# Optimization experiments

Measured on AMD Instinct MI355X. Metric: run time of the kernel, lower is better.

The kernel has to match this reference:

```python
import jax, jax.numpy as jnp
import numpy as np

EPS = 1e-5  # torch InstanceNorm3d default eps


def setup_inputs() -> dict:
    key = jax.random.key(0)
    ks = jax.random.split(key, 7)
    B, C, H, W, D = 2, 128, 48, 48, 48
    c_m, c_n = 128, 64
    return {
        "x": jax.random.normal(ks[0], (B, C, H, W, D), dtype=jnp.float32),
        "WA": jax.random.normal(ks[1], (c_m, C), dtype=jnp.float32) * (1.0 / np.sqrt(C)),
        "bA": jax.random.normal(ks[2], (c_m,), dtype=jnp.float32) * 0.01,
        "WB": jax.random.normal(ks[3], (c_n, C), dtype=jnp.float32) * (1.0 / np.sqrt(C)),
        "bB": jax.random.normal(ks[4], (c_n,), dtype=jnp.float32) * 0.01,
        "WV": jax.random.normal(ks[5], (c_n, C), dtype=jnp.float32) * (1.0 / np.sqrt(C)),
        "bV": jax.random.normal(ks[6], (c_n,), dtype=jnp.float32) * 0.01,
    }


def reference(x, WA, bA, WB, bB, WV, bV):
    B, C, H, W, D = x.shape
    L = H * W * D
    xf = x.reshape(B, C, L)
    # 1x1x1 Conv3d projections == per-voxel linear over channels
    A = jnp.einsum('bcl,mc->bml', xf, WA) + bA[None, :, None]   # (B, c_m, L)
    Bm = jnp.einsum('bcl,nc->bnl', xf, WB) + bB[None, :, None]  # (B, c_n, L)
    V = jnp.einsum('bcl,nc->bnl', xf, WV) + bV[None, :, None]   # (B, c_n, L)
    # attention maps: softmax over spatial positions
    attn_maps = jax.nn.softmax(Bm, axis=-1)                     # (B, c_n, L)
    # global descriptors: A @ attn_maps^T
    G = jnp.einsum('bml,bnl->bmn', A, attn_maps)                # (B, c_m, c_n)
    # attention vectors: softmax over c_n (channel) dim
    attn_vec = jax.nn.softmax(V, axis=1)                        # (B, c_n, L)
    Z = jnp.einsum('bmn,bnl->bml', G, attn_vec)                 # (B, c_m, L)
    # InstanceNorm3d (affine=False, biased variance) per (batch, channel)
    mean = jnp.mean(Z, axis=-1, keepdims=True)
    var = jnp.var(Z, axis=-1, keepdims=True)
    Zn = (Z - mean) * jax.lax.rsqrt(var + EPS)
    return Zn.reshape(B, Z.shape[1], H, W, D)
```

## Files before the change

### kernel.cpp

```cpp
#include <hip/hip_runtime.h>

#define LTOT 110592
#define EPSV 1e-5f

typedef _Float16 f16;
typedef __attribute__((ext_vector_type(4))) _Float16 f16x4;
typedef __attribute__((ext_vector_type(8))) _Float16 f16x8;
typedef __attribute__((ext_vector_type(4))) float f32x4;

#define MFMA16(a, b, c) __builtin_amdgcn_mfma_f32_16x16x32_f16(a, b, c, 0, 0, 0)
#define SWC(c) ((((c) ^ ((c) >> 3)) & 7) << 3)

__device__ __forceinline__ f16x8 ld_w8(const float* p) {
  const float4 a = *(const float4*)p;
  const float4 b = *(const float4*)(p + 4);
  f16x8 f;
  f[0] = (f16)a.x; f[1] = (f16)a.y; f[2] = (f16)a.z; f[3] = (f16)a.w;
  f[4] = (f16)b.x; f[5] = (f16)b.y; f[6] = (f16)b.z; f[7] = (f16)b.w;
  return f;
}

__global__ __launch_bounds__(256, 2) void p1_proj_m(
    const float* __restrict__ x,
    const float* __restrict__ WB_, const float* __restrict__ bB_,
    const float* __restrict__ WV_, const float* __restrict__ bV_,
    f16* __restrict__ av_g, f16* __restrict__ mpart, float* __restrict__ separt)
{
  __shared__ __align__(16) f16 XT[64 * 128 + 2240];
  __shared__ __align__(16) f16 XC[128 * 64];
  __shared__ __align__(16) f16 EL[64 * 64];
  __shared__ __align__(16) f16 AVT[64 * 64];
  __shared__ float colp[4][64];
  const int tid = threadIdx.x, b = blockIdx.y, blk = blockIdx.x;
  const int ln = tid & 63, w = tid >> 6, g = ln >> 4;

  const int nB = w * 16 + (ln & 15);
  f16x8 wbf[4], wvf[4];
  #pragma unroll
  for (int ks = 0; ks < 4; ++ks) {
    wbf[ks] = ld_w8(&WB_[nB * 128 + ks * 32 + g * 8]);
    wvf[ks] = ld_w8(&WV_[nB * 128 + ks * 32 + g * 8]);
  }
  const float sB = bB_[nB];
  float biasV[4];
  #pragma unroll
  for (int r = 0; r < 4; ++r) biasV[r] = bV_[w * 16 + g * 4 + r];

  f32x4 macc[8];
  #pragma unroll
  for (int i = 0; i < 8; ++i) macc[i] = (f32x4){0.f, 0.f, 0.f, 0.f};
  float se = 0.f;

  const int co = tid >> 4, LQ = tid & 15;
  const size_t xb = (size_t)b * 128 * LTOT;

  float4 xr[8];
  {
    const int l0 = blk * 256;
    #pragma unroll
    for (int j = 0; j < 8; ++j)
      xr[j] = *(const float4*)&x[xb + (size_t)(co * 8 + j) * LTOT + l0 + LQ * 4];
  }

  for (int t = 0; t < 4; ++t) {
    const int l0 = (blk * 4 + t) * 64;
    __syncthreads();
    #pragma unroll
    for (int i = 0; i < 4; ++i) {
      const int l = LQ * 4 + i;
      f16x8 v;
      #pragma unroll
      for (int j = 0; j < 8; ++j) v[j] = (f16)(((const float*)&xr[j])[i]);
      *(f16x8*)&XT[l * 128 + ((co * 8) ^ ((l & 7) << 3))] = v;
    }
    #pragma unroll
    for (int j = 0; j < 8; ++j) {
      const int c = co * 8 + j;
      f16x4 q;
      q[0] = (f16)xr[j].x; q[1] = (f16)xr[j].y;
      q[2] = (f16)xr[j].z; q[3] = (f16)xr[j].w;
      *(f16x4*)&XC[c * 64 + ((LQ * 4) ^ SWC(c))] = q;
    }
    __syncthreads();
    if (t < 3) {
      const int l0n = l0 + 64;
      #pragma unroll
      for (int j = 0; j < 8; ++j)
        xr[j] = *(const float4*)&x[xb + (size_t)(co * 8 + j) * LTOT + l0n + LQ * 4];
    }
    f32x4 aB[4], aV[4];
    #pragma unroll
    for (int lt = 0; lt < 4; ++lt) {
      aB[lt] = (f32x4){0.f, 0.f, 0.f, 0.f};
      aV[lt] = (f32x4){0.f, 0.f, 0.f, 0.f};
      const int l = lt * 16 + (ln & 15);
      #pragma unroll
      for (int ks = 0; ks < 4; ++ks) {
        const f16x8 xf = *(const f16x8*)&XT[l * 128 + (((ks * 4 + g) * 8) ^ ((l & 7) << 3))];
        aB[lt] = MFMA16(xf, wbf[ks], aB[lt]);
        aV[lt] = MFMA16(wvf[ks], xf, aV[lt]);
      }
    }
    #pragma unroll
    for (int lt = 0; lt < 4; ++lt) {
      f16x4 ev4;
      #pragma unroll
      for (int r = 0; r < 4; ++r) {
        const float e = __expf(aB[lt][r] + sB);
        se += e;
        ev4[r] = (f16)e;
      }
      const int lq = lt * 16 + g * 4;
      *(f16x4*)&EL[nB * 64 + (lq ^ ((nB & 7) << 3))] = ev4;
    }
    float cs[4];
    #pragma unroll
    for (int ct = 0; ct < 4; ++ct) {
      f16x4 av4;
      float s = 0.f;
      #pragma unroll
      for (int r = 0; r < 4; ++r) {
        const float e = __expf(aV[ct][r] + biasV[r]);
        s += e;
        av4[r] = (f16)e;
      }
      cs[ct] = s;
      const int l = ct * 16 + (ln & 15);
      *(f16x4*)&AVT[l * 64 + ((w * 16 + g * 4) ^ ((l & 7) << 3))] = av4;
    }
    #pragma unroll
    for (int ct = 0; ct < 4; ++ct) {
      cs[ct] += __shfl_xor(cs[ct], 16);
      cs[ct] += __shfl_xor(cs[ct], 32);
    }
    {
      const float v = (g == 0) ? cs[0] : (g == 1) ? cs[1] : (g == 2) ? cs[2] : cs[3];
      colp[w][g * 16 + (ln & 15)] = v;
    }
    __syncthreads();
    {
      const int l = tid >> 2, q = tid & 3;
      const float rs = 1.f / (colp[0][l] + colp[1][l] + colp[2][l] + colp[3][l]);
      f16x8 a0 = *(const f16x8*)&AVT[l * 64 + ((q * 16) ^ ((l & 7) << 3))];
      f16x8 a1 = *(const f16x8*)&AVT[l * 64 + ((q * 16 + 8) ^ ((l & 7) << 3))];
      #pragma unroll
      for (int j = 0; j < 8; ++j) {
        a0[j] = (f16)((float)a0[j] * rs);
        a1[j] = (f16)((float)a1[j] * rs);
      }
      f16* gp = av_g + ((size_t)b * LTOT + l0 + l) * 64 + q * 16;
      *(f16x8*)&gp[0] = a0;
      *(f16x8*)&gp[8] = a1;
    }
    {
      f16x8 el[2];
      #pragma unroll
      for (int ks = 0; ks < 2; ++ks)
        el[ks] = *(const f16x8*)&EL[nB * 64 + ((ks * 32 + g * 8) ^ ((nB & 7) << 3))];
      #pragma unroll
      for (int cblk = 0; cblk < 8; ++cblk) {
        const int c = cblk * 16 + (ln & 15);
        #pragma unroll
        for (int ks = 0; ks < 2; ++ks) {
          const f16x8 xcf = *(const f16x8*)&XC[c * 64 + ((ks * 32 + g * 8) ^ SWC(c))];
          macc[cblk] = MFMA16(el[ks], xcf, macc[cblk]);
        }
      }
    }
  }
  f16* mp = mpart + (size_t)(b * 432 + blk) * 8192;
  #pragma unroll
  for (int cblk = 0; cblk < 8; ++cblk)
    #pragma unroll
    for (int r = 0; r < 4; ++r)
      mp[(w * 16 + g * 4 + r) * 128 + cblk * 16 + (ln & 15)] = (f16)macc[cblk][r];
  se += __shfl_xor(se, 16);
  se += __shfl_xor(se, 32);
  if (ln < 16) separt[(size_t)(b * 432 + blk) * 64 + w * 16 + ln] = se;
}

__global__ __launch_bounds__(256, 2) void ka_red_cov(
    const f16* __restrict__ mpart, const float* __restrict__ separt,
    float* __restrict__ mpart2, float* __restrict__ sesum,
    const f16* __restrict__ av_g, f16* __restrict__ cpart,
    float* __restrict__ mupart)
{
  __shared__ __align__(16) f16 AV[64 * 64];
  const int bxa = blockIdx.x, b = blockIdx.y, tid = threadIdx.x;
  if (bxa < 257) {
    const int bx = bxa;
    if (bx < 256) {
      const int seg = bx >> 5, chunk = bx & 31;
      const int idx = chunk * 256 + tid;
      float s = 0.f;
      for (int j = 0; j < 54; ++j)
        s += (float)mpart[(size_t)(b * 432 + seg * 54 + j) * 8192 + idx];
      mpart2[(size_t)(b * 8 + seg) * 8192 + idx] = s;
    } else if (tid < 64) {
      float s = 0.f;
      for (int k = 0; k < 432; ++k) s += separt[(size_t)(b * 432 + k) * 64 + tid];
      sesum[b * 64 + tid] = s;
    }
    return;
  }
  const int blk = bxa - 257;
  const int ln = tid & 63, w = tid >> 6, g = ln >> 4;
  const int nq4 = (tid & 15) * 4, lq4 = (tid >> 4) * 4;
  const int nmu = tid >> 2, qmu = tid & 3;

  f32x4 cacc[4];
  #pragma unroll
  for (int j = 0; j < 4; ++j) cacc[j] = (f32x4){0.f, 0.f, 0.f, 0.f};
  float muacc = 0.f;

  for (int t = 0; t < 8; ++t) {
    const int l0 = (blk * 8 + t) * 64;
    __syncthreads();
    {
      f16x4 rd[4];
      #pragma unroll
      for (int i = 0; i < 4; ++i)
        rd[i] = *(const f16x4*)&av_g[((size_t)b * LTOT + l0 + lq4 + i) * 64 + nq4];
      #pragma unroll
      for (int j = 0; j < 4; ++j) {
        const int n = nq4 + j;
        f16x4 wr;
        #pragma unroll
        for (int i = 0; i < 4; ++i) wr[i] = rd[i][j];
        *(f16x4*)&AV[n * 64 + (lq4 ^ ((n & 7) << 3))] = wr;
      }
    }
    __syncthreads();
    {
      const f16x8 a0 = *(const f16x8*)&AV[nmu * 64 + ((qmu * 16) ^ ((nmu & 7) << 3))];
      const f16x8 a1 = *(const f16x8*)&AV[nmu * 64 + ((qmu * 16 + 8) ^ ((nmu & 7) << 3))];
      #pragma unroll
      for (int j = 0; j < 8; ++j) muacc += (float)a0[j] + (float)a1[j];
    }
    const int nA = w * 16 + (ln & 15);
    f16x8 caf[2];
    #pragma unroll
    for (int ks = 0; ks < 2; ++ks)
      caf[ks] = *(const f16x8*)&AV[nA * 64 + ((ks * 32 + g * 8) ^ ((nA & 7) << 3))];
    #pragma unroll
    for (int nct = 0; nct < 4; ++nct) {
      const int nb = nct * 16 + (ln & 15);
      #pragma unroll
      for (int ks = 0; ks < 2; ++ks) {
        const f16x8 cbf = *(const f16x8*)&AV[nb * 64 + ((ks * 32 + g * 8) ^ ((nb & 7) << 3))];
        cacc[nct] = MFMA16(caf[ks], cbf, cacc[nct]);
      }
    }
  }
  f16* cp = cpart + (size_t)(b * 216 + blk) * 4096;
  #pragma unroll
  for (int nct = 0; nct < 4; ++nct)
    #pragma unroll
    for (int r = 0; r < 4; ++r)
      cp[(w * 16 + g * 4 + r) * 64 + nct * 16 + (ln & 15)] = (f16)cacc[nct][r];
  muacc += __shfl_xor(muacc, 1);
  muacc += __shfl_xor(muacc, 2);
  if (qmu == 0) mupart[(size_t)(b * 216 + blk) * 64 + nmu] = muacc;
}

__global__ void kb_red(const float* __restrict__ mpart2, float* __restrict__ msum,
                       const f16* __restrict__ cpart, const float* __restrict__ mupart,
                       float* __restrict__ csum, float* __restrict__ musum)
{
  const int bxa = blockIdx.x, b = blockIdx.y, tid = threadIdx.x;
  if (bxa < 32) {
    const int idx = bxa * 256 + tid;
    float s = 0.f;
    #pragma unroll
    for (int k = 0; k < 8; ++k) s += mpart2[(size_t)(b * 8 + k) * 8192 + idx];
    msum[(size_t)b * 8192 + idx] = s;
    return;
  }
  const int bx = bxa - 32;
  if (bx < 64) {
    const int idx = bx * 64 + (tid >> 2), q = tid & 3;
    float s = 0.f;
    for (int k = q; k < 216; k += 4) s += (float)cpart[(size_t)(b * 216 + k) * 4096 + idx];
    s += __shfl_xor(s, 1);
    s += __shfl_xor(s, 2);
    if (q == 0) csum[(size_t)b * 4096 + idx] = s;
  } else if (tid < 64) {
    float s = 0.f;
    for (int k = 0; k < 216; ++k) s += mupart[(size_t)(b * 216 + k) * 64 + tid];
    musum[b * 64 + tid] = s;
  }
}

__global__ void p2b(const float* __restrict__ WA_, const float* __restrict__ bA_,
                    const float* __restrict__ msum, const float* __restrict__ sesum,
                    float* __restrict__ g32, f16* __restrict__ g16)
{
  const int b = blockIdx.y;
  const int idx = blockIdx.x * 256 + threadIdx.x;
  const int m = idx >> 6, n = idx & 63;
  float s = 0.f;
  #pragma unroll 4
  for (int c = 0; c < 128; ++c) s += WA_[m * 128 + c] * msum[(size_t)b * 8192 + n * 128 + c];
  const float gv = s / sesum[b * 64 + n] + bA_[m];
  g32[(size_t)b * 8192 + m * 64 + n] = gv;
  g16[(size_t)b * 8192 + m * 64 + (n ^ ((m & 7) << 3))] = (f16)gv;
}

__global__ void p4b(const float* __restrict__ csum, const float* __restrict__ musum,
                    const float* __restrict__ g32, float* __restrict__ mr)
{
  __shared__ __align__(16) float CL[4096];
  __shared__ __align__(16) float GLs[32 * 68];
  __shared__ float MUL[64];
  const int tid = threadIdx.x, b = blockIdx.y, bx = blockIdx.x;
  #pragma unroll
  for (int k = 0; k < 16; ++k) CL[k * 256 + tid] = csum[(size_t)b * 4096 + k * 256 + tid];
  #pragma unroll
  for (int k = 0; k < 8; ++k) {
    const int idx = k * 256 + tid;
    const int m_ = idx >> 6, n_ = idx & 63;
    GLs[m_ * 68 + n_] = g32[(size_t)b * 8192 + (bx * 32 + m_) * 64 + n_];
  }
  if (tid < 64) MUL[tid] = musum[b * 64 + tid];
  __syncthreads();
  const int mrow = (tid >> 3) * 68, oct = tid & 7;
  float q = 0.f;
  #pragma unroll
  for (int q4 = 0; q4 < 2; ++q4) {
    const int npb = oct * 8 + q4 * 4;
    float t0 = 0.f, t1 = 0.f, t2 = 0.f, t3 = 0.f;
    #pragma unroll 8
    for (int n = 0; n < 64; ++n) {
      const float4 cv = *(const float4*)&CL[n * 64 + npb];
      const float gv = GLs[mrow + n];
      t0 += gv * cv.x; t1 += gv * cv.y; t2 += gv * cv.z; t3 += gv * cv.w;
    }
    const float4 gq = *(const float4*)&GLs[mrow + npb];
    q += t0 * gq.x + t1 * gq.y + t2 * gq.z + t3 * gq.w;
  }
  q += __shfl_xor(q, 1); q += __shfl_xor(q, 2); q += __shfl_xor(q, 4);
  if (oct == 0) {
    float meanq = 0.f;
    #pragma unroll 8
    for (int n = 0; n < 64; ++n) meanq += GLs[mrow + n] * MUL[n];
    const int m = bx * 32 + (tid >> 3);
    const float mean = meanq / (float)LTOT;
    const float var = fmaxf(q / (float)LTOT - mean * mean, 0.f);
    mr[(b * 128 + m) * 2] = mean;
    mr[(b * 128 + m) * 2 + 1] = rsqrtf(var + EPSV);
  }
}

__global__ __launch_bounds__(256, 2) void p5_z(
    const f16* __restrict__ av_g, const f16* __restrict__ g16,
    const float* __restrict__ mr, float* __restrict__ out)
{
  __shared__ __align__(16) f16 AVT[64 * 64];
  const int tid = threadIdx.x, b = blockIdx.y, blk = blockIdx.x;
  const int ln = tid & 63, w = tid >> 6, g = ln >> 4;
  const int lst = tid & 63, pst = tid >> 6;

  f16x8 gf[2][2];
  float mean_[2][4], rsig_[2][4];
  #pragma unroll
  for (int mct = 0; mct < 2; ++mct) {
    const int mA = w * 32 + mct * 16 + (ln & 15);
    #pragma unroll
    for (int ks = 0; ks < 2; ++ks)
      gf[mct][ks] = *(const f16x8*)&g16[(size_t)b * 8192 + mA * 64 +
                                        (((ks * 4 + g) * 8) ^ ((mA & 7) << 3))];
    #pragma unroll
    for (int r = 0; r < 4; ++r) {
      const int m = w * 32 + mct * 16 + g * 4 + r;
      mean_[mct][r] = mr[(b * 128 + m) * 2];
      rsig_[mct][r] = mr[(b * 128 + m) * 2 + 1];
    }
  }

  for (int t = 0; t < 4; ++t) {
    const int l0 = (blk * 4 + t) * 64;
    __syncthreads();
    {
      const f16* gp = av_g + ((size_t)b * LTOT + l0 + lst) * 64 + pst * 16;
      const f16x8 a0 = *(const f16x8*)&gp[0];
      const f16x8 a1 = *(const f16x8*)&gp[8];
      *(f16x8*)&AVT[lst * 64 + ((pst * 16) ^ ((lst & 7) << 3))] = a0;
      *(f16x8*)&AVT[lst * 64 + ((pst * 16 + 8) ^ ((lst & 7) << 3))] = a1;
    }
    __syncthreads();
    #pragma unroll
    for (int lt = 0; lt < 4; ++lt) {
      const int l = lt * 16 + (ln & 15);
      f16x8 avf[2];
      #pragma unroll
      for (int ks = 0; ks < 2; ++ks)
        avf[ks] = *(const f16x8*)&AVT[l * 64 + (((ks * 4 + g) * 8) ^ ((l & 7) << 3))];
      #pragma unroll
      for (int mct = 0; mct < 2; ++mct) {
        f32x4 z = {0.f, 0.f, 0.f, 0.f};
        #pragma unroll
        for (int ks = 0; ks < 2; ++ks) z = MFMA16(gf[mct][ks], avf[ks], z);
        #pragma unroll
        for (int r = 0; r < 4; ++r) {
          const int m = w * 32 + mct * 16 + g * 4 + r;
          out[(size_t)(b * 128 + m) * LTOT + l0 + l] =
              (z[r] - mean_[mct][r]) * rsig_[mct][r];
        }
      }
    }
  }
}

extern "C" void kernel_launch(void* const* d_in, const int* in_sizes, int n_in,
                              void* d_out, int out_size, void* d_ws, size_t ws_size,
                              hipStream_t stream)
{
  const float* x  = (const float*)d_in[0];
  const float* WA = (const float*)d_in[1];
  const float* bA = (const float*)d_in[2];
  const float* WB = (const float*)d_in[3];
  const float* bB = (const float*)d_in[4];
  const float* WV = (const float*)d_in[5];
  const float* bV = (const float*)d_in[6];
  float* out = (float*)d_out;

  float* w = (float*)d_ws;
  f16*   mpart  = (f16*)w;
  float* mpart2 = w + 7077888;
  float* separt = mpart2 + 131072;
  float* msum   = separt + 55296;
  float* sesum  = msum + 16384;
  float* g32    = sesum + 128;
  f16*   g16f   = (f16*)(g32 + 16384);
  f16*   av_g   = g16f + 16384;
  f16*   cpart  = (f16*)(av_g + 14155776);
  float* mupart = (float*)(av_g + 14155776) + 1769472;
  float* csum   = mupart + 27648;
  float* musum  = csum + 8192;
  float* mr     = musum + 128;

  p1_proj_m<<<dim3(432, 2), 256, 0, stream>>>(x, WB, bB, WV, bV, av_g, mpart, separt);
  ka_red_cov<<<dim3(473, 2), 256, 0, stream>>>(mpart, separt, mpart2, sesum,
                                               av_g, cpart, mupart);
  kb_red<<<dim3(97, 2), 256, 0, stream>>>(mpart2, msum, cpart, mupart, csum, musum);
  p2b<<<dim3(32, 2), 256, 0, stream>>>(WA, bA, msum, sesum, g32, g16f);
  p4b<<<dim3(4, 2), 256, 0, stream>>>(csum, musum, g32, mr);
  p5_z<<<dim3(432, 2), 256, 0, stream>>>(av_g, g16f, mr, out);
}
```

Measured before the change: 110.3 us.

## Split p1 projection work across 512 threads with halved per-wave tiles

The first projection kernel now runs 512 threads per block. Each pair of waves shares one 16-row n slice and splits the spatial tiles and the channel blocks of the m accumulation between them. Per-thread register arrays (x prefetch, accumulators) are halved, which is meant to raise occupancy and latency hiding. The cost is more waves per block and doubled separt partial output, with the reduction and workspace offsets adjusted to match.

```diff
diff --git a/kernel.cpp b/kernel.cpp
--- a/kernel.cpp
+++ b/kernel.cpp
@@ -20,7 +20,7 @@
   return f;
 }
 
-__global__ __launch_bounds__(256, 2) void p1_proj_m(
+__global__ __launch_bounds__(512, 2) void p1_proj_m(
     const float* __restrict__ x,
     const float* __restrict__ WB_, const float* __restrict__ bB_,
     const float* __restrict__ WV_, const float* __restrict__ bV_,
@@ -33,8 +33,9 @@
   __shared__ float colp[4][64];
   const int tid = threadIdx.x, b = blockIdx.y, blk = blockIdx.x;
   const int ln = tid & 63, w = tid >> 6, g = ln >> 4;
-
-  const int nB = w * 16 + (ln & 15);
+  const int wn = w >> 1, h = w & 1;
+
+  const int nB = wn * 16 + (ln & 15);
   f16x8 wbf[4], wvf[4];
   #pragma unroll
   for (int ks = 0; ks < 4; ++ks) {
@@ -44,22 +45,22 @@
   const float sB = bB_[nB];
   float biasV[4];
   #pragma unroll
-  for (int r = 0; r < 4; ++r) biasV[r] = bV_[w * 16 + g * 4 + r];
-
-  f32x4 macc[8];
-  #pragma unroll
-  for (int i = 0; i < 8; ++i) macc[i] = (f32x4){0.f, 0.f, 0.f, 0.f};
+  for (int r = 0; r < 4; ++r) biasV[r] = bV_[wn * 16 + g * 4 + r];
+
+  f32x4 macc[4];
+  #pragma unroll
+  for (int i = 0; i < 4; ++i) macc[i] = (f32x4){0.f, 0.f, 0.f, 0.f};
   float se = 0.f;
 
-  const int co = tid >> 4, LQ = tid & 15;
+  const int cg = tid >> 4, LQ = tid & 15;
   const size_t xb = (size_t)b * 128 * LTOT;
 
-  float4 xr[8];
+  float4 xr[4];
   {
     const int l0 = blk * 256;
     #pragma unroll
-    for (int j = 0; j < 8; ++j)
-      xr[j] = *(const float4*)&x[xb + (size_t)(co * 8 + j) * LTOT + l0 + LQ * 4];
+    for (int j = 0; j < 4; ++j)
+      xr[j] = *(const float4*)&x[xb + (size_t)(cg * 4 + j) * LTOT + l0 + LQ * 4];
   }
 
   for (int t = 0; t < 4; ++t) {
@@ -68,14 +69,14 @@
     #pragma unroll
     for (int i = 0; i < 4; ++i) {
       const int l = LQ * 4 + i;
-      f16x8 v;
-      #pragma unroll
-      for (int j = 0; j < 8; ++j) v[j] = (f16)(((const float*)&xr[j])[i]);
-      *(f16x8*)&XT[l * 128 + ((co * 8) ^ ((l & 7) << 3))] = v;
-    }
-    #pragma unroll
-    for (int j = 0; j < 8; ++j) {
-      const int c = co * 8 + j;
+      f16x4 v;
+      #pragma unroll
+      for (int j = 0; j < 4; ++j) v[j] = (f16)(((const float*)&xr[j])[i]);
+      *(f16x4*)&XT[l * 128 + ((cg * 4) ^ ((l & 7) << 3))] = v;
+    }
+    #pragma unroll
+    for (int j = 0; j < 4; ++j) {
+      const int c = cg * 4 + j;
       f16x4 q;
       q[0] = (f16)xr[j].x; q[1] = (f16)xr[j].y;
       q[2] = (f16)xr[j].z; q[3] = (f16)xr[j].w;
@@ -85,72 +86,63 @@
     if (t < 3) {
       const int l0n = l0 + 64;
       #pragma unroll
-      for (int j = 0; j < 8; ++j)
-        xr[j] = *(const float4*)&x[xb + (size_t)(co * 8 + j) * LTOT + l0n + LQ * 4];
-    }
-    f32x4 aB[4], aV[4];
-    #pragma unroll
-    for (int lt = 0; lt < 4; ++lt) {
-      aB[lt] = (f32x4){0.f, 0.f, 0.f, 0.f};
-      aV[lt] = (f32x4){0.f, 0.f, 0.f, 0.f};
-      const int l = lt * 16 + (ln & 15);
+      for (int j = 0; j < 4; ++j)
+        xr[j] = *(const float4*)&x[xb + (size_t)(cg * 4 + j) * LTOT + l0n + LQ * 4];
+    }
+    f32x4 aB[2], aV[2];
+    #pragma unroll
+    for (int u = 0; u < 2; ++u) {
+      aB[u] = (f32x4){0.f, 0.f, 0.f, 0.f};
+      aV[u] = (f32x4){0.f, 0.f, 0.f, 0.f};
+      const int l = (2 * h + u) * 16 + (ln & 15);
       #pragma unroll
       for (int ks = 0; ks < 4; ++ks) {
         const f16x8 xf = *(const f16x8*)&XT[l * 128 + (((ks * 4 + g) * 8) ^ ((l & 7) << 3))];
-        aB[lt] = MFMA16(xf, wbf[ks], aB[lt]);
-        aV[lt] = MFMA16(wvf[ks], xf, aV[lt]);
-      }
-    }
-    #pragma unroll
-    for (int lt = 0; lt < 4; ++lt) {
+        aB[u] = MFMA16(xf, wbf[ks], aB[u]);
+        aV[u] = MFMA16(wvf[ks], xf, aV[u]);
+      }
+    }
+    #pragma unroll
+    for (int u = 0; u < 2; ++u) {
       f16x4 ev4;
       #pragma unroll
       for (int r = 0; r < 4; ++r) {
-        const float e = __expf(aB[lt][r] + sB);
+        const float e = __expf(aB[u][r] + sB);
         se += e;
         ev4[r] = (f16)e;
       }
-      const int lq = lt * 16 + g * 4;
+      const int lq = (2 * h + u) * 16 + g * 4;
       *(f16x4*)&EL[nB * 64 + (lq ^ ((nB & 7) << 3))] = ev4;
     }
-    float cs[4];
-    #pragma unroll
-    for (int ct = 0; ct < 4; ++ct) {
+    float cs[2];
+    #pragma unroll
+    for (int u = 0; u < 2; ++u) {
       f16x4 av4;
       float s = 0.f;
       #pragma unroll
       for (int r = 0; r < 4; ++r) {
-        const float e = __expf(aV[ct][r] + biasV[r]);
+        const float e = __expf(aV[u][r] + biasV[r]);
         s += e;
         av4[r] = (f16)e;
       }
-      cs[ct] = s;
-      const int l = ct * 16 + (ln & 15);
-      *(f16x4*)&AVT[l * 64 + ((w * 16 + g * 4) ^ ((l & 7) << 3))] = av4;
-    }
-    #pragma unroll
-    for (int ct = 0; ct < 4; ++ct) {
-      cs[ct] += __shfl_xor(cs[ct], 16);
-      cs[ct] += __shfl_xor(cs[ct], 32);
-    }
+      cs[u] = s;
+      const int l = (2 * h + u) * 16 + (ln & 15);
+      *(f16x4*)&AVT[l * 64 + ((wn * 16 + g * 4) ^ ((l & 7) << 3))] = av4;
+    }
+    #pragma unroll
+    for (int u = 0; u < 2; ++u) {
+      cs[u] += __shfl_xor(cs[u], 16);
+      cs[u] += __shfl_xor(cs[u], 32);
+    }
+    if (g < 2) colp[wn][(2 * h + g) * 16 + (ln & 15)] = cs[g & 1];
+    __syncthreads();
     {
-      const float v = (g == 0) ? cs[0] : (g == 1) ? cs[1] : (g == 2) ? cs[2] : cs[3];
-      colp[w][g * 16 + (ln & 15)] = v;
-    }
-    __syncthreads();
-    {
-      const int l = tid >> 2, q = tid & 3;
+      const int l = tid >> 3, q = tid & 7;
       const float rs = 1.f / (colp[0][l] + colp[1][l] + colp[2][l] + colp[3][l]);
-      f16x8 a0 = *(const f16x8*)&AVT[l * 64 + ((q * 16) ^ ((l & 7) << 3))];
-      f16x8 a1 = *(const f16x8*)&AVT[l * 64 + ((q * 16 + 8) ^ ((l & 7) << 3))];
-      #pragma unroll
-      for (int j = 0; j < 8; ++j) {
-        a0[j] = (f16)((float)a0[j] * rs);
-        a1[j] = (f16)((float)a1[j] * rs);
-      }
-      f16* gp = av_g + ((size_t)b * LTOT + l0 + l) * 64 + q * 16;
-      *(f16x8*)&gp[0] = a0;
-      *(f16x8*)&gp[8] = a1;
+      f16x8 a0 = *(const f16x8*)&AVT[l * 64 + ((q * 8) ^ ((l & 7) << 3))];
+      #pragma unroll
+      for (int j = 0; j < 8; ++j) a0[j] = (f16)((float)a0[j] * rs);
+      *(f16x8*)&av_g[((size_t)b * LTOT + l0 + l) * 64 + q * 8] = a0;
     }
     {
       f16x8 el[2];
@@ -158,25 +150,26 @@
       for (int ks = 0; ks < 2; ++ks)
         el[ks] = *(const f16x8*)&EL[nB * 64 + ((ks * 32 + g * 8) ^ ((nB & 7) << 3))];
       #pragma unroll
-      for (int cblk = 0; cblk < 8; ++cblk) {
-        const int c = cblk * 16 + (ln & 15);
+      for (int cb = 0; cb < 4; ++cb) {
+        const int c = (h * 4 + cb) * 16 + (ln & 15);
         #pragma unroll
         for (int ks = 0; ks < 2; ++ks) {
           const f16x8 xcf = *(const f16x8*)&XC[c * 64 + ((ks * 32 + g * 8) ^ SWC(c))];
-          macc[cblk] = MFMA16(el[ks], xcf, macc[cblk]);
+          macc[cb] = MFMA16(el[ks], xcf, macc[cb]);
         }
       }
     }
   }
   f16* mp = mpart + (size_t)(b * 432 + blk) * 8192;
   #pragma unroll
-  for (int cblk = 0; cblk < 8; ++cblk)
+  for (int cb = 0; cb < 4; ++cb)
     #pragma unroll
     for (int r = 0; r < 4; ++r)
-      mp[(w * 16 + g * 4 + r) * 128 + cblk * 16 + (ln & 15)] = (f16)macc[cblk][r];
+      mp[(wn * 16 + g * 4 + r) * 128 + (h * 4 + cb) * 16 + (ln & 15)] = (f16)macc[cb][r];
   se += __shfl_xor(se, 16);
   se += __shfl_xor(se, 32);
-  if (ln < 16) separt[(size_t)(b * 432 + blk) * 64 + w * 16 + ln] = se;
+  if (ln < 16)
+    separt[(size_t)(b * 432 + blk) * 128 + h * 64 + wn * 16 + ln] = se;
 }
 
 __global__ __launch_bounds__(256, 2) void ka_red_cov(
@@ -198,7 +191,10 @@
       mpart2[(size_t)(b * 8 + seg) * 8192 + idx] = s;
     } else if (tid < 64) {
       float s = 0.f;
-      for (int k = 0; k < 432; ++k) s += separt[(size_t)(b * 432 + k) * 64 + tid];
+      for (int k = 0; k < 432; ++k) {
+        const float* sp = &separt[(size_t)(b * 432 + k) * 128];
+        s += sp[tid] + sp[64 + tid];
+      }
       sesum[b * 64 + tid] = s;
     }
     return;
@@ -428,7 +424,7 @@
   f16*   mpart  = (f16*)w;
   float* mpart2 = w + 7077888;
   float* separt = mpart2 + 131072;
-  float* msum   = separt + 55296;
+  float* msum   = separt + 110592;
   float* sesum  = msum + 16384;
   float* g32    = sesum + 128;
   f16*   g16f   = (f16*)(g32 + 16384);
@@ -439,7 +435,7 @@
   float* musum  = csum + 8192;
   float* mr     = musum + 128;
 
-  p1_proj_m<<<dim3(432, 2), 256, 0, stream>>>(x, WB, bB, WV, bV, av_g, mpart, separt);
+  p1_proj_m<<<dim3(432, 2), 512, 0, stream>>>(x, WB, bB, WV, bV, av_g, mpart, separt);
   ka_red_cov<<<dim3(473, 2), 256, 0, stream>>>(mpart, separt, mpart2, sesum,
                                                av_g, cpart, mupart);
   kb_red<<<dim3(97, 2), 256, 0, stream>>>(mpart2, msum, cpart, mupart, csum, musum);
```

Result: slower. 130.0 us (+17.9%).
